# Kernel optimization log

Hardware: AMD Instinct MI355X
Metric: run time of the kernel (lower is better)

## Reference

```python
import jax, jax.numpy as jnp
import numpy as np

B, S, D = 4, 2048, 1024


def setup_inputs() -> dict:
    key = jax.random.key(0)
    kx, kq, kk, kv, km = jax.random.split(key, 5)
    x = jax.random.normal(kx, (B, S, D), dtype=jnp.float32)
    # bias-free Linear weights, torch convention W: (out, in), y = x @ W.T
    Wq = jax.random.normal(kq, (D, D), dtype=jnp.float32) * 0.02
    Wk = jax.random.normal(kk, (D, D), dtype=jnp.float32) * 0.02
    Wv = jax.random.normal(kv, (D, D), dtype=jnp.float32) * 0.02
    # quantum mask: probability vector per batch over seq positions
    q_mask = jax.nn.softmax(jax.random.normal(km, (B, S), dtype=jnp.float32), axis=-1)
    return {"x": x, "Wq": Wq, "Wk": Wk, "Wv": Wv, "q_mask": q_mask}


def reference(x, Wq, Wk, Wv, q_mask):
    # projections (torch Linear: x @ W.T)
    q = jnp.einsum("bsd,ed->bse", x, Wq)
    k = jnp.einsum("bsd,ed->bse", x, Wk)
    v = jnp.einsum("bsd,ed->bse", x, Wv)
    scale = 1.0 / jnp.sqrt(jnp.asarray(D, dtype=x.dtype))
    scores = jnp.einsum("bqe,bke->bqk", q, k) * scale  # (B, S, S)
    # per-row multiplicative quantum mask (mask broadcast over key dim)
    scores = scores * q_mask[:, :, None]
    attn = jax.nn.softmax(scores, axis=-1)
    out = jnp.einsum("bqk,bkd->bqd", attn, v)
    return out
```

## Files before the change

kernel.cpp:

```cpp
#include <hip/hip_runtime.h>
#include <hip/hip_bf16.h>

#define BB 4
#define SS 2048
#define DD 1024

using f32x4  = __attribute__((ext_vector_type(4))) float;
using f32x16 = __attribute__((ext_vector_type(16))) float;
using i32x4  = __attribute__((ext_vector_type(4))) int;
using i32x8  = __attribute__((ext_vector_type(8))) int;

struct f8_t { unsigned char b; };

__device__ __forceinline__ void gld16(const void* g, void* l) {
    __builtin_amdgcn_global_load_lds(
        (const __attribute__((address_space(1))) void*)(g),
        (__attribute__((address_space(3))) void*)(l),
        16, 0, 0);
}

__device__ __forceinline__ void store1(float* p, float v) { *p = v; }
__device__ __forceinline__ void store1(f8_t* p, float v)  {
    p->b = (unsigned char)(__builtin_amdgcn_cvt_pk_fp8_f32(v, v, 0, false) & 0xff);
}

__global__ void cvt_x_kernel(const float* __restrict__ x, unsigned char* __restrict__ x8, int n8) {
    int i = blockIdx.x * blockDim.x + threadIdx.x;
    if (i >= n8) return;
    float4 a = ((const float4*)x)[2 * i];
    float4 b = ((const float4*)x)[2 * i + 1];
    int lo = __builtin_amdgcn_cvt_pk_fp8_f32(a.x, a.y, 0, false);
    lo     = __builtin_amdgcn_cvt_pk_fp8_f32(a.z, a.w, lo, true);
    int hi = __builtin_amdgcn_cvt_pk_fp8_f32(b.x, b.y, 0, false);
    hi     = __builtin_amdgcn_cvt_pk_fp8_f32(b.z, b.w, hi, true);
    ((int2*)x8)[i] = make_int2(lo, hi);
}

__global__ void cvt_w_kernel(const float* __restrict__ Wq, const float* __restrict__ Wk,
                             const float* __restrict__ Wv, unsigned char* __restrict__ w8, int n8) {
    int i = blockIdx.x * blockDim.x + threadIdx.x;
    int seg = i / n8;
    int j = i - seg * n8;
    const float* src = (seg == 0) ? Wq : (seg == 1) ? Wk : Wv;
    float4 a = ((const float4*)src)[2 * j];
    float4 b = ((const float4*)src)[2 * j + 1];
    int lo = __builtin_amdgcn_cvt_pk_fp8_f32(a.x, a.y, 0, false);
    lo     = __builtin_amdgcn_cvt_pk_fp8_f32(a.z, a.w, lo, true);
    int hi = __builtin_amdgcn_cvt_pk_fp8_f32(b.x, b.y, 0, false);
    hi     = __builtin_amdgcn_cvt_pk_fp8_f32(b.z, b.w, hi, true);
    ((int2*)(w8 + (size_t)seg * n8 * 8))[j] = make_int2(lo, hi);
}

__global__ void xsum_kernel(const float* __restrict__ x, float* __restrict__ xsum) {
    int bd = blockIdx.x;
    int b  = bd >> 2, dc = bd & 3;
    int d  = dc * 256 + threadIdx.x;
    int s0 = blockIdx.y * 128;
    const float* p = x + ((size_t)b * SS + s0) * DD + d;
    float acc = 0.f;
    for (int i = 0; i < 128; ++i) acc += p[(size_t)i * DD];
    atomicAdd(&xsum[b * DD + d], acc);
}

__global__ void colsumv_kernel(const float* __restrict__ Wv, const float* __restrict__ xsum,
                               float* __restrict__ colsum) {
    int idx  = blockIdx.x * 4 + (threadIdx.x >> 6);
    int b    = idx >> 10, c = idx & 1023;
    int lane = threadIdx.x & 63;
    const float* wr = Wv + (size_t)c * DD;
    const float* xs = xsum + b * DD;
    float acc = 0.f;
#pragma unroll 4
    for (int d = lane; d < DD; d += 64) acc += wr[d] * xs[d];
#pragma unroll
    for (int off = 32; off; off >>= 1) acc += __shfl_xor(acc, off);
    if (lane == 0) colsum[idx] = acc;
}

template <int MODE, typename CT>
__global__ __launch_bounds__(256, 4) void gemm_f8(
    const unsigned char* __restrict__ A, const unsigned char* __restrict__ B,
    CT* __restrict__ C, int M, int N, int K,
    long batchA, long batchB, long batchC,
    int ldc, int col_shift, long cstride,
    const float* __restrict__ qmask, float* __restrict__ rsum,
    const float* __restrict__ colsum) {
    constexpr int BM = 128, BN = 128, BK = 128;
    constexpr int SCALE_A = (MODE == 3) ? 118 : 127;
    __shared__ __attribute__((aligned(16))) unsigned char As[BM * BK];
    __shared__ __attribute__((aligned(16))) unsigned char Bs[BN * BK];

    const int tid  = threadIdx.x;
    const int lane = tid & 63;
    const int wv   = tid >> 6;
    const int l31  = lane & 31;
    const int half = lane >> 5;
    const int hb   = half * 2;
    const int wm   = wv >> 1;
    const int wn   = wv & 1;

    const int m0 = blockIdx.y * BM;
    const int n0 = blockIdx.x * BN;
    const long z = blockIdx.z;
    const unsigned char* Ab = A + z * batchA;
    const unsigned char* Bb = B + z * batchB;

    f32x16 acc[2][2] = {};

#define STAGE(dst, src, kt, j) do {                                           \
        int slot_ = (j) * 256 + tid;                                          \
        int r_ = slot_ >> 3;                                                  \
        int c_ = (slot_ & 7) ^ (r_ & 7);                                      \
        gld16((src) + (size_t)r_ * K + ((kt) + c_ * 16),                      \
              (dst) + (size_t)((j) * 256 + wv * 64) * 16);                    \
    } while (0)
#define RDFRAG(f, base, rr, s) do {                                           \
        int r_ = (rr);                                                        \
        int c0_ = (s) * 4 + hb;                                               \
        const unsigned char* rp_ = (base) + r_ * 128;                         \
        i32x4 q0_ = *(const i32x4*)(rp_ + ((c0_ ^ (r_ & 7)) * 16));           \
        i32x4 q1_ = *(const i32x4*)(rp_ + (((c0_ + 1) ^ (r_ & 7)) * 16));     \
        f[0]=q0_[0]; f[1]=q0_[1]; f[2]=q0_[2]; f[3]=q0_[3];                   \
        f[4]=q1_[0]; f[5]=q1_[1]; f[6]=q1_[2]; f[7]=q1_[3];                   \
    } while (0)
#define MFMA(d, a, b) \
        d = __builtin_amdgcn_mfma_scale_f32_32x32x64_f8f6f4(a, b, d, 0, 0, 0, SCALE_A, 0, 127)

    for (int kt = 0; kt < K; kt += BK) {
        STAGE(As, Ab + (size_t)m0 * K, kt, 0); STAGE(As, Ab + (size_t)m0 * K, kt, 1);
        STAGE(As, Ab + (size_t)m0 * K, kt, 2); STAGE(As, Ab + (size_t)m0 * K, kt, 3);
        STAGE(Bs, Bb + (size_t)n0 * K, kt, 0); STAGE(Bs, Bb + (size_t)n0 * K, kt, 1);
        STAGE(Bs, Bb + (size_t)n0 * K, kt, 2); STAGE(Bs, Bb + (size_t)n0 * K, kt, 3);
        asm volatile("s_waitcnt vmcnt(0)" ::: "memory");
        __syncthreads();

#pragma unroll
        for (int s = 0; s < 2; ++s) {
            i32x8 a0, a1, b0, b1;
            RDFRAG(a0, As, wm * 64 +  0 + l31, s);
            RDFRAG(a1, As, wm * 64 + 32 + l31, s);
            RDFRAG(b0, Bs, wn * 64 +  0 + l31, s);
            RDFRAG(b1, Bs, wn * 64 + 32 + l31, s);
            MFMA(acc[0][0], a0, b0); MFMA(acc[0][1], a0, b1);
            MFMA(acc[1][0], a1, b0); MFMA(acc[1][1], a1, b1);
        }
        __syncthreads();
    }
#undef STAGE
#undef RDFRAG
#undef MFMA

    CT* Cb = C + z * batchC;

    if constexpr (MODE == 0) {
#pragma unroll
        for (int mi = 0; mi < 2; ++mi)
#pragma unroll
            for (int ni = 0; ni < 2; ++ni) {
                int colg = n0 + wn * 64 + ni * 32 + l31;
#pragma unroll
                for (int reg = 0; reg < 16; ++reg) {
                    int rowg = m0 + wm * 64 + mi * 32 + (reg & 3) + 8 * (reg >> 2) + 4 * half;
                    store1(Cb + (size_t)rowg * ldc + colg, acc[mi][ni][reg]);
                }
            }
    } else if constexpr (MODE == 1) {
#pragma unroll
        for (int mi = 0; mi < 2; ++mi)
#pragma unroll
            for (int ni = 0; ni < 2; ++ni) {
                int colg = n0 + wn * 64 + ni * 32 + l31;
                int cb   = colg >> col_shift;
                int ccol = colg - (cb << col_shift);
#pragma unroll
                for (int reg = 0; reg < 16; ++reg) {
                    int rowg = m0 + wm * 64 + mi * 32 + (reg & 3) + 8 * (reg >> 2) + 4 * half;
                    store1(Cb + (long)cb * cstride + (size_t)rowg * ldc + ccol, acc[mi][ni][reg]);
                }
            }
    } else if constexpr (MODE == 2) {
        const float* qm = qmask + (z << 11);
        float* rs = rsum + (z << 11);
#pragma unroll
        for (int mi = 0; mi < 2; ++mi) {
#pragma unroll
            for (int reg = 0; reg < 16; ++reg) {
                int rowg = m0 + wm * 64 + mi * 32 + (reg & 3) + 8 * (reg >> 2) + 4 * half;
                float fac = qm[rowg] * 0.03125f;
                float part = 0.f;
#pragma unroll
                for (int ni = 0; ni < 2; ++ni) {
                    int colg = n0 + wn * 64 + ni * 32 + l31;
                    float t = __expf(acc[mi][ni][reg] * fac) - 1.0f;
                    part += t;
                    store1(Cb + (size_t)rowg * ldc + colg, t * 512.0f);
                }
                part += __shfl_xor(part, 1);
                part += __shfl_xor(part, 2);
                part += __shfl_xor(part, 4);
                part += __shfl_xor(part, 8);
                part += __shfl_xor(part, 16);
                if (l31 == 0) atomicAdd(&rs[rowg], part);
            }
        }
    } else {
        const float* rs = rsum + (z << 11);
        const float* cs = colsum + (z << 10);
#pragma unroll
        for (int mi = 0; mi < 2; ++mi) {
#pragma unroll
            for (int reg = 0; reg < 16; ++reg) {
                int rowg = m0 + wm * 64 + mi * 32 + (reg & 3) + 8 * (reg >> 2) + 4 * half;
                float inv = 1.0f / (2048.0f + rs[rowg]);
#pragma unroll
                for (int ni = 0; ni < 2; ++ni) {
                    int colg = n0 + wn * 64 + ni * 32 + l31;
                    store1(Cb + (size_t)rowg * ldc + colg, (acc[mi][ni][reg] + cs[colg]) * inv);
                }
            }
        }
    }
}

extern "C" void kernel_launch(void* const* d_in, const int* in_sizes, int n_in,
                              void* d_out, int out_size, void* d_ws, size_t ws_size,
                              hipStream_t stream) {
    const float* x     = (const float*)d_in[0];
    const float* Wq    = (const float*)d_in[1];
    const float* Wk    = (const float*)d_in[2];
    const float* Wv    = (const float*)d_in[3];
    const float* qmask = (const float*)d_in[4];
    float* out = (float*)d_out;

    const long nx = (long)BB * SS * DD;
    const long nw = (long)DD * DD;

    unsigned char* ws  = (unsigned char*)d_ws;
    unsigned char* x8  = ws;
    unsigned char* w8  = x8 + nx;
    unsigned char* qk8 = w8 + 3 * nw;
    unsigned char* vt8 = qk8 + 2 * nx;
    unsigned char* t8  = vt8 + nx;
    float* xsum   = (float*)(t8 + (long)BB * SS * SS);
    float* rs     = xsum + BB * DD;
    float* colsum = rs + BB * SS;

    hipMemsetAsync(xsum, 0, (size_t)(BB * DD + BB * SS) * sizeof(float), stream);

    cvt_x_kernel<<<dim3((int)(nx / 8 / 256)), dim3(256), 0, stream>>>(x, x8, (int)(nx / 8));
    cvt_w_kernel<<<dim3((int)(3 * nw / 8 / 256)), dim3(256), 0, stream>>>(Wq, Wk, Wv, w8, (int)(nw / 8));
    xsum_kernel<<<dim3(16, 16), dim3(256), 0, stream>>>(x, xsum);
    colsumv_kernel<<<dim3(1024), dim3(256), 0, stream>>>(Wv, xsum, colsum);

    gemm_f8<0, f8_t><<<dim3(DD / 128, (BB * SS) / 128, 2), 256, 0, stream>>>(
        x8, w8, (f8_t*)qk8, BB * SS, DD, DD, 0, nw, nx, DD, 31, 0, nullptr, nullptr, nullptr);

    gemm_f8<1, f8_t><<<dim3((BB * SS) / 128, DD / 128, 1), 256, 0, stream>>>(
        w8 + 2 * nw, x8, (f8_t*)vt8, DD, BB * SS, DD, 0, 0, 0, SS, 11, (long)DD * SS,
        nullptr, nullptr, nullptr);

    gemm_f8<2, f8_t><<<dim3(SS / 128, SS / 128, BB), 256, 0, stream>>>(
        qk8, qk8 + nx, (f8_t*)t8, SS, SS, DD, (long)SS * DD, (long)SS * DD, (long)SS * SS,
        SS, 31, 0, qmask, rs, nullptr);

    gemm_f8<3, float><<<dim3(DD / 128, SS / 128, BB), 256, 0, stream>>>(
        t8, vt8, out, SS, DD, SS, (long)SS * SS, (long)DD * SS, (long)SS * DD,
        DD, 31, 0, nullptr, rs, colsum);
}
```

Before: 214.5 us.

## Add 256x256 fp8 GEMM kernel with interleaved prefetch for QK projection and scores

Adds a new gemm_f8_big kernel with 256x256x128 tiles, 512 threads and 16x16x128 scaled fp8 MFMA. It interleaves the global-to-LDS prefetch of the next K tile with the MFMA phases, using barriers and setprio. The QK projection and the score/exp GEMM now use this kernel, which raises data reuse per block and overlaps loads with compute. The cost is more registers (a 128-float accumulator), heavy LDS use, fewer blocks per launch, and more barriers per iteration.

```diff
diff --git a/kernel.cpp b/kernel.cpp
--- a/kernel.cpp
+++ b/kernel.cpp
@@ -152,19 +152,7 @@
 
     CT* Cb = C + z * batchC;
 
-    if constexpr (MODE == 0) {
-#pragma unroll
-        for (int mi = 0; mi < 2; ++mi)
-#pragma unroll
-            for (int ni = 0; ni < 2; ++ni) {
-                int colg = n0 + wn * 64 + ni * 32 + l31;
-#pragma unroll
-                for (int reg = 0; reg < 16; ++reg) {
-                    int rowg = m0 + wm * 64 + mi * 32 + (reg & 3) + 8 * (reg >> 2) + 4 * half;
-                    store1(Cb + (size_t)rowg * ldc + colg, acc[mi][ni][reg]);
-                }
-            }
-    } else if constexpr (MODE == 1) {
+    if constexpr (MODE == 1) {
 #pragma unroll
         for (int mi = 0; mi < 2; ++mi)
 #pragma unroll
@@ -178,45 +166,186 @@
                     store1(Cb + (long)cb * cstride + (size_t)rowg * ldc + ccol, acc[mi][ni][reg]);
                 }
             }
-    } else if constexpr (MODE == 2) {
+    } else {
+        const float* rs = rsum + (z << 11);
+        const float* cs = colsum + (z << 10);
+#pragma unroll
+        for (int mi = 0; mi < 2; ++mi) {
+#pragma unroll
+            for (int reg = 0; reg < 16; ++reg) {
+                int rowg = m0 + wm * 64 + mi * 32 + (reg & 3) + 8 * (reg >> 2) + 4 * half;
+                float inv = 1.0f / (2048.0f + rs[rowg]);
+#pragma unroll
+                for (int ni = 0; ni < 2; ++ni) {
+                    int colg = n0 + wn * 64 + ni * 32 + l31;
+                    store1(Cb + (size_t)rowg * ldc + colg, (acc[mi][ni][reg] + cs[colg]) * inv);
+                }
+            }
+        }
+    }
+}
+
+template <int MODE, typename CT>
+__global__ __launch_bounds__(512, 2) void gemm_f8_big(
+    const unsigned char* __restrict__ A, const unsigned char* __restrict__ B,
+    CT* __restrict__ C, int K,
+    long batchA, long batchB, long batchC, int ldc,
+    const float* __restrict__ qmask, float* __restrict__ rsum) {
+    constexpr int BM = 256, BN = 256, BK = 128;
+    __shared__ __attribute__((aligned(16))) unsigned char As[2][BM * BK];
+    __shared__ __attribute__((aligned(16))) unsigned char Bs[2][BN * BK];
+
+    const int tid  = threadIdx.x;
+    const int lane = tid & 63;
+    const int wv   = tid >> 6;
+    const int l16  = lane & 15;
+    const int quad = lane >> 4;
+    const int wm   = wv >> 2;
+    const int wn   = wv & 3;
+
+    const int m0 = blockIdx.y * BM;
+    const int n0 = blockIdx.x * BN;
+    const long z = blockIdx.z;
+    const unsigned char* Ab = A + z * batchA;
+    const unsigned char* Bb = B + z * batchB;
+
+    const int cbase = 2 * quad;
+
+    f32x4 acc[8][4] = {};
+
+#define STA(buf, kt, j) do {                                                  \
+        int slot_ = (j) * 512 + tid;                                          \
+        int r_ = slot_ >> 3;                                                  \
+        int c_ = (slot_ & 7) ^ (r_ & 7);                                      \
+        gld16(Ab + (size_t)(m0 + r_) * K + ((kt) + c_ * 16),                  \
+              &As[buf][((j) * 512 + wv * 64) * 16]);                          \
+    } while (0)
+#define STB(buf, kt, j) do {                                                  \
+        int slot_ = (j) * 512 + tid;                                          \
+        int r_ = slot_ >> 3;                                                  \
+        int c_ = (slot_ & 7) ^ (r_ & 7);                                      \
+        gld16(Bb + (size_t)(n0 + r_) * K + ((kt) + c_ * 16),                  \
+              &Bs[buf][((j) * 512 + wv * 64) * 16]);                          \
+    } while (0)
+#define RD(f, base, r) do {                                                   \
+        int cc_ = cbase ^ ((r) & 7);                                          \
+        i32x4 p0_ = *(const i32x4*)((base) + (r) * 128 + cc_ * 16);           \
+        i32x4 p1_ = *(const i32x4*)((base) + (r) * 128 + (cc_ ^ 1) * 16);     \
+        f[0]=p0_[0]; f[1]=p0_[1]; f[2]=p0_[2]; f[3]=p0_[3];                   \
+        f[4]=p1_[0]; f[5]=p1_[1]; f[6]=p1_[2]; f[7]=p1_[3];                   \
+    } while (0)
+#define MM(d, a, b) \
+        d = __builtin_amdgcn_mfma_scale_f32_16x16x128_f8f6f4(a, b, d, 0, 0, 0, 127, 0, 127)
+#define LGKM0() do { \
+        asm volatile("s_waitcnt lgkmcnt(0)" ::: "memory"); \
+        __builtin_amdgcn_sched_barrier(0); } while (0)
+
+    STA(0, 0, 0); STA(0, 0, 1); STA(0, 0, 2); STA(0, 0, 3);
+    STB(0, 0, 0); STB(0, 0, 1); STB(0, 0, 2); STB(0, 0, 3);
+    asm volatile("s_waitcnt vmcnt(0)" ::: "memory");
+    __builtin_amdgcn_s_barrier();
+
+    const int NT = K / BK;
+    for (int t = 0; t < NT; ++t) {
+        const int cur = t & 1;
+        const int nxt = cur ^ 1;
+        const unsigned char* Ac = &As[cur][0];
+        const unsigned char* Bc = &Bs[cur][0];
+        const int ktn = (t + 1) * BK;
+        const bool pf = (t + 1 < NT);
+
+        i32x8 b0, b1, b2, b3, aA, aB;
+
+        RD(b0, Bc, wn * 64 +  0 + l16);
+        RD(b1, Bc, wn * 64 + 16 + l16);
+        RD(b2, Bc, wn * 64 + 32 + l16);
+        RD(b3, Bc, wn * 64 + 48 + l16);
+        RD(aA, Ac, wm * 128 +  0 + l16);
+        RD(aB, Ac, wm * 128 + 16 + l16);
+        if (pf) { STA(nxt, ktn, 0); STA(nxt, ktn, 1); STA(nxt, ktn, 2); }
+        __builtin_amdgcn_s_barrier();
+        LGKM0();
+        __builtin_amdgcn_s_setprio(1);
+        MM(acc[0][0], aA, b0); MM(acc[0][1], aA, b1); MM(acc[0][2], aA, b2); MM(acc[0][3], aA, b3);
+        MM(acc[1][0], aB, b0); MM(acc[1][1], aB, b1); MM(acc[1][2], aB, b2); MM(acc[1][3], aB, b3);
+        __builtin_amdgcn_s_setprio(0);
+        __builtin_amdgcn_s_barrier();
+
+        RD(aA, Ac, wm * 128 + 32 + l16);
+        RD(aB, Ac, wm * 128 + 48 + l16);
+        if (pf) { STA(nxt, ktn, 3); STB(nxt, ktn, 0); STB(nxt, ktn, 1); }
+        __builtin_amdgcn_s_barrier();
+        LGKM0();
+        __builtin_amdgcn_s_setprio(1);
+        MM(acc[2][0], aA, b0); MM(acc[2][1], aA, b1); MM(acc[2][2], aA, b2); MM(acc[2][3], aA, b3);
+        MM(acc[3][0], aB, b0); MM(acc[3][1], aB, b1); MM(acc[3][2], aB, b2); MM(acc[3][3], aB, b3);
+        __builtin_amdgcn_s_setprio(0);
+        __builtin_amdgcn_s_barrier();
+
+        RD(aA, Ac, wm * 128 + 64 + l16);
+        RD(aB, Ac, wm * 128 + 80 + l16);
+        if (pf) { STB(nxt, ktn, 2); STB(nxt, ktn, 3); }
+        __builtin_amdgcn_s_barrier();
+        LGKM0();
+        __builtin_amdgcn_s_setprio(1);
+        MM(acc[4][0], aA, b0); MM(acc[4][1], aA, b1); MM(acc[4][2], aA, b2); MM(acc[4][3], aA, b3);
+        MM(acc[5][0], aB, b0); MM(acc[5][1], aB, b1); MM(acc[5][2], aB, b2); MM(acc[5][3], aB, b3);
+        __builtin_amdgcn_s_setprio(0);
+        __builtin_amdgcn_s_barrier();
+
+        RD(aA, Ac, wm * 128 +  96 + l16);
+        RD(aB, Ac, wm * 128 + 112 + l16);
+        __builtin_amdgcn_s_barrier();
+        LGKM0();
+        __builtin_amdgcn_s_setprio(1);
+        MM(acc[6][0], aA, b0); MM(acc[6][1], aA, b1); MM(acc[6][2], aA, b2); MM(acc[6][3], aA, b3);
+        MM(acc[7][0], aB, b0); MM(acc[7][1], aB, b1); MM(acc[7][2], aB, b2); MM(acc[7][3], aB, b3);
+        __builtin_amdgcn_s_setprio(0);
+        asm volatile("s_waitcnt vmcnt(0)" ::: "memory");
+        __builtin_amdgcn_s_barrier();
+    }
+#undef STA
+#undef STB
+#undef RD
+#undef MM
+#undef LGKM0
+
+    CT* Cb = C + z * batchC;
+
+    if constexpr (MODE == 0) {
+#pragma unroll
+        for (int mi = 0; mi < 8; ++mi)
+#pragma unroll
+            for (int ni = 0; ni < 4; ++ni) {
+                int colg = n0 + wn * 64 + ni * 16 + l16;
+#pragma unroll
+                for (int r = 0; r < 4; ++r) {
+                    int rowg = m0 + wm * 128 + mi * 16 + quad * 4 + r;
+                    store1(Cb + (size_t)rowg * ldc + colg, acc[mi][ni][r]);
+                }
+            }
+    } else {
         const float* qm = qmask + (z << 11);
         float* rs = rsum + (z << 11);
 #pragma unroll
-        for (int mi = 0; mi < 2; ++mi) {
-#pragma unroll
-            for (int reg = 0; reg < 16; ++reg) {
-                int rowg = m0 + wm * 64 + mi * 32 + (reg & 3) + 8 * (reg >> 2) + 4 * half;
+        for (int mi = 0; mi < 8; ++mi) {
+#pragma unroll
+            for (int r = 0; r < 4; ++r) {
+                int rowg = m0 + wm * 128 + mi * 16 + quad * 4 + r;
                 float fac = qm[rowg] * 0.03125f;
                 float part = 0.f;
 #pragma unroll
-                for (int ni = 0; ni < 2; ++ni) {
-                    int colg = n0 + wn * 64 + ni * 32 + l31;
-                    float t = __expf(acc[mi][ni][reg] * fac) - 1.0f;
-                    part += t;
-                    store1(Cb + (size_t)rowg * ldc + colg, t * 512.0f);
+                for (int ni = 0; ni < 4; ++ni) {
+                    int colg = n0 + wn * 64 + ni * 16 + l16;
+                    float tt = __expf(acc[mi][ni][r] * fac) - 1.0f;
+                    part += tt;
+                    store1(Cb + (size_t)rowg * ldc + colg, tt * 512.0f);
                 }
                 part += __shfl_xor(part, 1);
                 part += __shfl_xor(part, 2);
                 part += __shfl_xor(part, 4);
                 part += __shfl_xor(part, 8);
-                part += __shfl_xor(part, 16);
-                if (l31 == 0) atomicAdd(&rs[rowg], part);
-            }
-        }
-    } else {
-        const float* rs = rsum + (z << 11);
-        const float* cs = colsum + (z << 10);
-#pragma unroll
-        for (int mi = 0; mi < 2; ++mi) {
-#pragma unroll
-            for (int reg = 0; reg < 16; ++reg) {
-                int rowg = m0 + wm * 64 + mi * 32 + (reg & 3) + 8 * (reg >> 2) + 4 * half;
-                float inv = 1.0f / (2048.0f + rs[rowg]);
-#pragma unroll
-                for (int ni = 0; ni < 2; ++ni) {
-                    int colg = n0 + wn * 64 + ni * 32 + l31;
-                    store1(Cb + (size_t)rowg * ldc + colg, (acc[mi][ni][reg] + cs[colg]) * inv);
-                }
+                if (l16 == 0) atomicAdd(&rs[rowg], part);
             }
         }
     }
@@ -252,16 +381,16 @@
     xsum_kernel<<<dim3(16, 16), dim3(256), 0, stream>>>(x, xsum);
     colsumv_kernel<<<dim3(1024), dim3(256), 0, stream>>>(Wv, xsum, colsum);
 
-    gemm_f8<0, f8_t><<<dim3(DD / 128, (BB * SS) / 128, 2), 256, 0, stream>>>(
-        x8, w8, (f8_t*)qk8, BB * SS, DD, DD, 0, nw, nx, DD, 31, 0, nullptr, nullptr, nullptr);
+    gemm_f8_big<0, f8_t><<<dim3(DD / 256, (BB * SS) / 256, 2), 512, 0, stream>>>(
+        x8, w8, (f8_t*)qk8, DD, 0, nw, nx, DD, nullptr, nullptr);
 
     gemm_f8<1, f8_t><<<dim3((BB * SS) / 128, DD / 128, 1), 256, 0, stream>>>(
         w8 + 2 * nw, x8, (f8_t*)vt8, DD, BB * SS, DD, 0, 0, 0, SS, 11, (long)DD * SS,
         nullptr, nullptr, nullptr);
 
-    gemm_f8<2, f8_t><<<dim3(SS / 128, SS / 128, BB), 256, 0, stream>>>(
-        qk8, qk8 + nx, (f8_t*)t8, SS, SS, DD, (long)SS * DD, (long)SS * DD, (long)SS * SS,
-        SS, 31, 0, qmask, rs, nullptr);
+    gemm_f8_big<2, f8_t><<<dim3(SS / 256, SS / 256, BB), 512, 0, stream>>>(
+        qk8, qk8 + nx, (f8_t*)t8, DD, (long)SS * DD, (long)SS * DD, (long)SS * SS,
+        SS, qmask, rs);
 
     gemm_f8<3, float><<<dim3(DD / 128, SS / 128, BB), 256, 0, stream>>>(
         t8, vt8, out, SS, DD, SS, (long)SS * SS, (long)DD * SS, (long)SS * DD,
```

New measurement: 212.6 us. About the same (-0.9%).

## Fuse x fp8 conversion with column-sum and double GEMM K-tile depth

Applied to the files above, without the earlier changes.

Merges the fp8 conversion of x with the per-batch sum over sequence positions into one kernel, so x is read from global memory once instead of twice and one launch disappears. Separately, the fp8 GEMM K tile grows from 128 to 256 with matching staging and swizzle changes, halving the number of barrier-synchronised load/compute iterations. The larger tile doubles LDS use to 64 KB per block and lowers the occupancy hint from 4 to 2 blocks, which reduces latency hiding since loads and MFMAs are still not overlapped.

```diff
diff --git a/kernel.cpp b/kernel.cpp
--- a/kernel.cpp
+++ b/kernel.cpp
@@ -24,16 +24,42 @@
     p->b = (unsigned char)(__builtin_amdgcn_cvt_pk_fp8_f32(v, v, 0, false) & 0xff);
 }
 
-__global__ void cvt_x_kernel(const float* __restrict__ x, unsigned char* __restrict__ x8, int n8) {
-    int i = blockIdx.x * blockDim.x + threadIdx.x;
-    if (i >= n8) return;
-    float4 a = ((const float4*)x)[2 * i];
-    float4 b = ((const float4*)x)[2 * i + 1];
-    int lo = __builtin_amdgcn_cvt_pk_fp8_f32(a.x, a.y, 0, false);
-    lo     = __builtin_amdgcn_cvt_pk_fp8_f32(a.z, a.w, lo, true);
-    int hi = __builtin_amdgcn_cvt_pk_fp8_f32(b.x, b.y, 0, false);
-    hi     = __builtin_amdgcn_cvt_pk_fp8_f32(b.z, b.w, hi, true);
-    ((int2*)x8)[i] = make_int2(lo, hi);
+__global__ void cvt_x_xsum_kernel(const float* __restrict__ x,
+                                  unsigned char* __restrict__ x8,
+                                  float* __restrict__ xsum) {
+    int b  = blockIdx.x >> 6;
+    int s0 = (blockIdx.x & 63) * 32;
+    int t  = threadIdx.x;
+    int g  = t >> 7;
+    int dt = t & 127;
+    int d8 = dt * 8;
+    const float* xb = x + ((size_t)b * SS + s0 + g * 16) * DD + d8;
+    unsigned char* x8b = x8 + ((size_t)b * SS + s0 + g * 16) * DD + d8;
+
+    float a0=0,a1=0,a2=0,a3=0,a4=0,a5=0,a6=0,a7=0;
+#pragma unroll 4
+    for (int i = 0; i < 16; ++i) {
+        float4 u = *(const float4*)(xb + (size_t)i * DD);
+        float4 v = *(const float4*)(xb + (size_t)i * DD + 4);
+        int lo = __builtin_amdgcn_cvt_pk_fp8_f32(u.x, u.y, 0, false);
+        lo     = __builtin_amdgcn_cvt_pk_fp8_f32(u.z, u.w, lo, true);
+        int hi = __builtin_amdgcn_cvt_pk_fp8_f32(v.x, v.y, 0, false);
+        hi     = __builtin_amdgcn_cvt_pk_fp8_f32(v.z, v.w, hi, true);
+        *(int2*)(x8b + (size_t)i * DD) = make_int2(lo, hi);
+        a0 += u.x; a1 += u.y; a2 += u.z; a3 += u.w;
+        a4 += v.x; a5 += v.y; a6 += v.z; a7 += v.w;
+    }
+    __shared__ float red[2][128][8];
+    float* r = red[g][dt];
+    r[0]=a0; r[1]=a1; r[2]=a2; r[3]=a3; r[4]=a4; r[5]=a5; r[6]=a6; r[7]=a7;
+    __syncthreads();
+    if (t < 128) {
+        float* p0 = red[0][t];
+        float* p1 = red[1][t];
+#pragma unroll
+        for (int j = 0; j < 8; ++j)
+            atomicAdd(&xsum[b * DD + t * 8 + j], p0[j] + p1[j]);
+    }
 }
 
 __global__ void cvt_w_kernel(const float* __restrict__ Wq, const float* __restrict__ Wk,
@@ -51,17 +77,6 @@
     ((int2*)(w8 + (size_t)seg * n8 * 8))[j] = make_int2(lo, hi);
 }
 
-__global__ void xsum_kernel(const float* __restrict__ x, float* __restrict__ xsum) {
-    int bd = blockIdx.x;
-    int b  = bd >> 2, dc = bd & 3;
-    int d  = dc * 256 + threadIdx.x;
-    int s0 = blockIdx.y * 128;
-    const float* p = x + ((size_t)b * SS + s0) * DD + d;
-    float acc = 0.f;
-    for (int i = 0; i < 128; ++i) acc += p[(size_t)i * DD];
-    atomicAdd(&xsum[b * DD + d], acc);
-}
-
 __global__ void colsumv_kernel(const float* __restrict__ Wv, const float* __restrict__ xsum,
                                float* __restrict__ colsum) {
     int idx  = blockIdx.x * 4 + (threadIdx.x >> 6);
@@ -78,14 +93,14 @@
 }
 
 template <int MODE, typename CT>
-__global__ __launch_bounds__(256, 4) void gemm_f8(
+__global__ __launch_bounds__(256, 2) void gemm_f8(
     const unsigned char* __restrict__ A, const unsigned char* __restrict__ B,
     CT* __restrict__ C, int M, int N, int K,
     long batchA, long batchB, long batchC,
     int ldc, int col_shift, long cstride,
     const float* __restrict__ qmask, float* __restrict__ rsum,
     const float* __restrict__ colsum) {
-    constexpr int BM = 128, BN = 128, BK = 128;
+    constexpr int BM = 128, BN = 128, BK = 256;
     constexpr int SCALE_A = (MODE == 3) ? 118 : 127;
     __shared__ __attribute__((aligned(16))) unsigned char As[BM * BK];
     __shared__ __attribute__((aligned(16))) unsigned char Bs[BN * BK];
@@ -109,15 +124,15 @@
 
 #define STAGE(dst, src, kt, j) do {                                           \
         int slot_ = (j) * 256 + tid;                                          \
-        int r_ = slot_ >> 3;                                                  \
-        int c_ = (slot_ & 7) ^ (r_ & 7);                                      \
+        int r_ = slot_ >> 4;                                                  \
+        int c_ = (slot_ & 15) ^ (r_ & 7);                                     \
         gld16((src) + (size_t)r_ * K + ((kt) + c_ * 16),                      \
               (dst) + (size_t)((j) * 256 + wv * 64) * 16);                    \
     } while (0)
 #define RDFRAG(f, base, rr, s) do {                                           \
         int r_ = (rr);                                                        \
         int c0_ = (s) * 4 + hb;                                               \
-        const unsigned char* rp_ = (base) + r_ * 128;                         \
+        const unsigned char* rp_ = (base) + r_ * 256;                         \
         i32x4 q0_ = *(const i32x4*)(rp_ + ((c0_ ^ (r_ & 7)) * 16));           \
         i32x4 q1_ = *(const i32x4*)(rp_ + (((c0_ + 1) ^ (r_ & 7)) * 16));     \
         f[0]=q0_[0]; f[1]=q0_[1]; f[2]=q0_[2]; f[3]=q0_[3];                   \
@@ -127,15 +142,21 @@
         d = __builtin_amdgcn_mfma_scale_f32_32x32x64_f8f6f4(a, b, d, 0, 0, 0, SCALE_A, 0, 127)
 
     for (int kt = 0; kt < K; kt += BK) {
-        STAGE(As, Ab + (size_t)m0 * K, kt, 0); STAGE(As, Ab + (size_t)m0 * K, kt, 1);
-        STAGE(As, Ab + (size_t)m0 * K, kt, 2); STAGE(As, Ab + (size_t)m0 * K, kt, 3);
-        STAGE(Bs, Bb + (size_t)n0 * K, kt, 0); STAGE(Bs, Bb + (size_t)n0 * K, kt, 1);
-        STAGE(Bs, Bb + (size_t)n0 * K, kt, 2); STAGE(Bs, Bb + (size_t)n0 * K, kt, 3);
+        const unsigned char* Asrc = Ab + (size_t)m0 * K;
+        const unsigned char* Bsrc = Bb + (size_t)n0 * K;
+        STAGE(As, Asrc, kt, 0); STAGE(As, Asrc, kt, 1);
+        STAGE(As, Asrc, kt, 2); STAGE(As, Asrc, kt, 3);
+        STAGE(As, Asrc, kt, 4); STAGE(As, Asrc, kt, 5);
+        STAGE(As, Asrc, kt, 6); STAGE(As, Asrc, kt, 7);
+        STAGE(Bs, Bsrc, kt, 0); STAGE(Bs, Bsrc, kt, 1);
+        STAGE(Bs, Bsrc, kt, 2); STAGE(Bs, Bsrc, kt, 3);
+        STAGE(Bs, Bsrc, kt, 4); STAGE(Bs, Bsrc, kt, 5);
+        STAGE(Bs, Bsrc, kt, 6); STAGE(Bs, Bsrc, kt, 7);
         asm volatile("s_waitcnt vmcnt(0)" ::: "memory");
         __syncthreads();
 
 #pragma unroll
-        for (int s = 0; s < 2; ++s) {
+        for (int s = 0; s < 4; ++s) {
             i32x8 a0, a1, b0, b1;
             RDFRAG(a0, As, wm * 64 +  0 + l31, s);
             RDFRAG(a1, As, wm * 64 + 32 + l31, s);
@@ -247,9 +268,8 @@
 
     hipMemsetAsync(xsum, 0, (size_t)(BB * DD + BB * SS) * sizeof(float), stream);
 
-    cvt_x_kernel<<<dim3((int)(nx / 8 / 256)), dim3(256), 0, stream>>>(x, x8, (int)(nx / 8));
+    cvt_x_xsum_kernel<<<dim3(256), dim3(256), 0, stream>>>(x, x8, xsum);
     cvt_w_kernel<<<dim3((int)(3 * nw / 8 / 256)), dim3(256), 0, stream>>>(Wq, Wk, Wv, w8, (int)(nw / 8));
-    xsum_kernel<<<dim3(16, 16), dim3(256), 0, stream>>>(x, xsum);
     colsumv_kernel<<<dim3(1024), dim3(256), 0, stream>>>(Wv, xsum, colsum);
 
     gemm_f8<0, f8_t><<<dim3(DD / 128, (BB * SS) / 128, 2), 256, 0, stream>>>(
```

After: 233.1 us. +8.7%, slower.
